# Kernel optimization log

Measured on AMD Instinct MI355X. Metric: run time of the kernel, lower is better.

The kernel has to match this reference:

```python
import jax, jax.numpy as jnp
import numpy as np

DIM = 512
NUM_HEADS = 8


def setup_inputs() -> dict:
    key = jax.random.key(0)
    k1, k2, k3, k4, k5 = jax.random.split(key, 5)
    B, N, C = 4, 4096, DIM
    x = jax.random.normal(k1, (B, N, C), dtype=jnp.float32)
    # Conv1d kernel_size=1 weights, squeezed to [out, in]
    qkv_w = jax.random.normal(k2, (3 * C, C), dtype=jnp.float32) * (C ** -0.5)
    qkv_b = jax.random.normal(k3, (3 * C,), dtype=jnp.float32) * 0.02
    out_w = jax.random.normal(k4, (C, C), dtype=jnp.float32) * (C ** -0.5)
    out_b = jax.random.normal(k5, (C,), dtype=jnp.float32) * 0.02
    return {"x": x, "qkv_w": qkv_w, "qkv_b": qkv_b, "out_w": out_w, "out_b": out_b}


def reference(x, qkv_w, qkv_b, out_w, out_b):
    B, N, C = x.shape
    H = NUM_HEADS
    hd = C // H
    scale = hd ** -0.5
    # 1x1 Conv1d == per-position linear: [B,N,C] x [3C,C] -> [B,N,3C]
    qkv = jnp.einsum('bnc,oc->bno', x, qkv_w) + qkv_b
    qkv = qkv.reshape(B, N, 3, H, hd)
    q, k, v = qkv[:, :, 0], qkv[:, :, 1], qkv[:, :, 2]  # each [B,N,H,hd]
    # NOTE: faithful to the original: q @ k.transpose(-2,-1) contracts head_dim
    # giving an [B,N,H,H] score matrix (attention across heads per position).
    scores = jnp.einsum('bnhd,bngd->bnhg', q, k) * scale
    attn = jax.nn.softmax(scores, axis=-1)
    out = jnp.einsum('bnhg,bngd->bnhd', attn, v)  # [B,N,H,hd]
    # Faithful to original: transpose(1,2) then reshape(B,N,C) interleaves axes.
    out = out.transpose(0, 2, 1, 3).reshape(B, N, C)
    out = jnp.einsum('bnc,oc->bno', out, out_w) + out_b
    return out
```

## Files before the change

### kernel.cpp

```cpp
#include <hip/hip_runtime.h>
#include <hip/hip_bf16.h>

#define DIMC 512
#define SEQ 4096
#define M_TOK 16384
#define N_QKV 1536

typedef __bf16 bfv8 __attribute__((ext_vector_type(8)));
typedef float f32v4 __attribute__((ext_vector_type(4)));
typedef unsigned short u16v8 __attribute__((ext_vector_type(8)));

#define VMCNT(n) asm volatile("s_waitcnt vmcnt(" #n ")" ::: "memory")
#define LGKM0()  asm volatile("s_waitcnt lgkmcnt(0)" ::: "memory")

static __device__ __forceinline__ float bf2f(unsigned short u) {
    union { unsigned int i; float f; } x; x.i = ((unsigned int)u) << 16; return x.f;
}
static __device__ __forceinline__ unsigned short f2bf(float f) {
    union { float f; unsigned int i; } x; x.f = f;
    unsigned int r = x.i + 0x7FFFu + ((x.i >> 16) & 1u);
    return (unsigned short)(r >> 16);
}

static __device__ __forceinline__ void gload_lds16(const void* g, void* s) {
    __builtin_amdgcn_global_load_lds(
        (const __attribute__((address_space(1))) unsigned int*)g,
        (__attribute__((address_space(3))) unsigned int*)s, 16, 0, 0);
}

#define NWQ8 (N_QKV * DIMC / 8)
#define NWO8 (DIMC * DIMC / 8)
__global__ __launch_bounds__(256) void cvt_w(
    const float* __restrict__ wq, const float* __restrict__ wo,
    unsigned short* __restrict__ wqb, unsigned short* __restrict__ wob)
{
    int i = blockIdx.x * 256 + threadIdx.x;
    const float* src; unsigned short* dst; int off;
    if (i < NWQ8) { src = wq; dst = wqb; off = i; }
    else          { src = wo; dst = wob; off = i - NWQ8; }
    const float4* p = (const float4*)src + (size_t)off * 2;
    float4 a = p[0], b = p[1];
    u16v8 o;
    o[0] = f2bf(a.x); o[1] = f2bf(a.y); o[2] = f2bf(a.z); o[3] = f2bf(a.w);
    o[4] = f2bf(b.x); o[5] = f2bf(b.y); o[6] = f2bf(b.z); o[7] = f2bf(b.w);
    *(u16v8*)(dst + (size_t)off * 8) = o;
}

__global__ __launch_bounds__(512) void gemm_qkv_f32a(
    const float* __restrict__ A,
    const unsigned short* __restrict__ B,
    const float* __restrict__ bias,
    unsigned short* __restrict__ Cout,
    int M, int N, int K)
{
    __shared__ __align__(16) unsigned short As[3][128 * 32];
    __shared__ __align__(16) unsigned short Bs[3][256 * 32];
    const int tid  = threadIdx.x;
    const int lane = tid & 63;
    const int wid  = tid >> 6;
    const int wm   = wid >> 2;
    const int wn   = wid & 3;
    const int m0 = blockIdx.x * 128;
    const int n0 = blockIdx.y * 256;
    const int frow = lane & 15;
    const int fcol = (lane >> 4) * 8;
    const int NT = K >> 5;

    f32v4 acc[4][4] = {};

    const int arow = wid * 16 + (lane & 15);
    const int ak0  = (lane >> 4) * 8;
    const float* aSrcF = A + (size_t)(m0 + arow) * K + ak0;
    const int aWidx = (arow * 32 + ak0) ^ (((arow >> 1) & 3) << 3);

    const unsigned short* bSrc[2];
    #pragma unroll
    for (int r = 0; r < 2; ++r) {
        const int brow = r * 128 + (tid >> 2);
        const int bcol = ((tid & 3) * 8) ^ (((brow >> 1) & 3) << 3);
        bSrc[r] = B + (size_t)(n0 + brow) * K + bcol;
    }
    const int bDst = wid * 512;

#define STAGE_B(kt, slot)                                                      \
    {                                                                          \
        gload_lds16(bSrc[0] + (kt) * 32, &Bs[slot][bDst]);                     \
        gload_lds16(bSrc[1] + (kt) * 32, &Bs[slot][4096 + bDst]);              \
    }
#define A_LOAD(kt, v0, v1)                                                     \
    { v0 = *(const float4*)(aSrcF + (kt) * 32);                                \
      v1 = *(const float4*)(aSrcF + (kt) * 32 + 4); }
#define A_WRITE(slot, v0, v1)                                                  \
    {                                                                          \
        u16v8 cv_;                                                             \
        cv_[0] = f2bf(v0.x); cv_[1] = f2bf(v0.y); cv_[2] = f2bf(v0.z);         \
        cv_[3] = f2bf(v0.w); cv_[4] = f2bf(v1.x); cv_[5] = f2bf(v1.y);         \
        cv_[6] = f2bf(v1.z); cv_[7] = f2bf(v1.w);                              \
        *(u16v8*)&As[slot][aWidx] = cv_;                                       \
    }

    float4 aC0, aC1, aN0, aN1, p00, p01, p10, p11;
    A_LOAD(0, p00, p01)
    A_LOAD(1, p10, p11)
    STAGE_B(0, 0)
    STAGE_B(1, 1)
    A_WRITE(0, p00, p01)
    A_WRITE(1, p10, p11)
    A_LOAD(2, aC0, aC1)
    VMCNT(4);
    LGKM0();
    __builtin_amdgcn_s_barrier();

    for (int t = 0; t < NT; ++t) {
        const int slot = t % 3;
        if (t + 3 < NT) A_LOAD(t + 3, aN0, aN1)
        if (t + 2 < NT) {
            STAGE_B(t + 2, (t + 2) % 3)
            A_WRITE((t + 2) % 3, aC0, aC1)
        }
        bfv8 af[4], bf[4];
        #pragma unroll
        for (int i = 0; i < 4; ++i) {
            const int r = wm * 64 + i * 16 + frow;
            af[i] = *(const bfv8*)(&As[slot][r * 32 + (fcol ^ (((r >> 1) & 3) << 3))]);
        }
        #pragma unroll
        for (int j = 0; j < 4; ++j) {
            const int r = wn * 64 + j * 16 + frow;
            bf[j] = *(const bfv8*)(&Bs[slot][r * 32 + (fcol ^ (((r >> 1) & 3) << 3))]);
        }
        LGKM0(); __builtin_amdgcn_sched_barrier(0);
        #pragma unroll
        for (int i = 0; i < 4; ++i)
            #pragma unroll
            for (int j = 0; j < 4; ++j)
                acc[i][j] = __builtin_amdgcn_mfma_f32_16x16x32_bf16(
                    af[i], bf[j], acc[i][j], 0, 0, 0);
        if (t + 2 < NT) { VMCNT(4); } else { VMCNT(0); }
        __builtin_amdgcn_s_barrier();
        aC0 = aN0; aC1 = aN1;
    }
#undef STAGE_B
#undef A_LOAD
#undef A_WRITE

    const int erow = (lane >> 4) * 4;
    const int ecol = lane & 15;
    #pragma unroll
    for (int j = 0; j < 4; ++j) {
        const int col = n0 + wn * 64 + j * 16 + ecol;
        const float bv = bias[col];
        #pragma unroll
        for (int i = 0; i < 4; ++i) {
            const int rbase = m0 + wm * 64 + i * 16 + erow;
            #pragma unroll
            for (int r = 0; r < 4; ++r)
                Cout[(size_t)(rbase + r) * N + col] = f2bf(acc[i][j][r] + bv);
        }
    }
}

__global__ __launch_bounds__(512) void gemm_nt_r3(
    const unsigned short* __restrict__ A,
    const unsigned short* __restrict__ B,
    const float* __restrict__ bias,
    float* __restrict__ Cout,
    int M, int N, int K)
{
    __shared__ __align__(16) unsigned short As[3][128 * 32];
    __shared__ __align__(16) unsigned short Bs[3][256 * 32];
    const int tid  = threadIdx.x;
    const int lane = tid & 63;
    const int wid  = tid >> 6;
    const int wm   = wid >> 2;
    const int wn   = wid & 3;
    const int m0 = blockIdx.x * 128;
    const int n0 = blockIdx.y * 256;
    const int frow = lane & 15;
    const int fcol = (lane >> 4) * 8;
    const int NT = K >> 5;

    f32v4 acc[4][4] = {};

    const int arow = tid >> 2;
    const int acol = ((tid & 3) * 8) ^ (((arow >> 1) & 3) << 3);
    const unsigned short* aSrc = A + (size_t)(m0 + arow) * K + acol;
    const unsigned short* bSrc[2];
    #pragma unroll
    for (int r = 0; r < 2; ++r) {
        const int brow = r * 128 + (tid >> 2);
        const int bcol = ((tid & 3) * 8) ^ (((brow >> 1) & 3) << 3);
        bSrc[r] = B + (size_t)(n0 + brow) * K + bcol;
    }
    const int aDst = wid * 512;

#define STAGE(kt, slot)                                                        \
    {                                                                          \
        gload_lds16(aSrc + (kt) * 32, &As[slot][aDst]);                        \
        gload_lds16(bSrc[0] + (kt) * 32, &Bs[slot][aDst]);                     \
        gload_lds16(bSrc[1] + (kt) * 32, &Bs[slot][4096 + aDst]);              \
    }

    STAGE(0, 0)
    STAGE(1, 1)
    VMCNT(3);
    __builtin_amdgcn_s_barrier();

    for (int t = 0; t < NT; ++t) {
        const int slot = t % 3;
        bfv8 af[4], bf[4];
        #pragma unroll
        for (int i = 0; i < 4; ++i) {
            const int r = wm * 64 + i * 16 + frow;
            af[i] = *(const bfv8*)(&As[slot][r * 32 + (fcol ^ (((r >> 1) & 3) << 3))]);
        }
        #pragma unroll
        for (int j = 0; j < 4; ++j) {
            const int r = wn * 64 + j * 16 + frow;
            bf[j] = *(const bfv8*)(&Bs[slot][r * 32 + (fcol ^ (((r >> 1) & 3) << 3))]);
        }
        if (t + 2 < NT) STAGE(t + 2, (t + 2) % 3)
        LGKM0(); __builtin_amdgcn_sched_barrier(0);
        #pragma unroll
        for (int i = 0; i < 4; ++i)
            #pragma unroll
            for (int j = 0; j < 4; ++j)
                acc[i][j] = __builtin_amdgcn_mfma_f32_16x16x32_bf16(
                    af[i], bf[j], acc[i][j], 0, 0, 0);
        if (t + 2 < NT) { VMCNT(3); } else { VMCNT(0); }
        __builtin_amdgcn_s_barrier();
    }
#undef STAGE

    const int erow = (lane >> 4) * 4;
    const int ecol = lane & 15;
    #pragma unroll
    for (int j = 0; j < 4; ++j) {
        const int col = n0 + wn * 64 + j * 16 + ecol;
        const float bv = bias[col];
        #pragma unroll
        for (int i = 0; i < 4; ++i) {
            const int rbase = m0 + wm * 64 + i * 16 + erow;
            #pragma unroll
            for (int r = 0; r < 4; ++r)
                Cout[(size_t)(rbase + r) * N + col] = acc[i][j][r] + bv;
        }
    }
}

__global__ __launch_bounds__(256) void attn_mix2(
    const unsigned short* __restrict__ Y1,
    unsigned short* __restrict__ Y2)
{
    const int tid  = threadIdx.x;
    const int tok  = blockIdx.x * 16 + (tid >> 4);
    const int l16  = tid & 15;
    const int h    = l16 >> 1;
    const int half = l16 & 1;
    const unsigned short* qkv = Y1 + (size_t)tok * N_QKV;

    float qf[32];
    #pragma unroll
    for (int c = 0; c < 4; ++c) {
        u16v8 v = *(const u16v8*)(qkv + h * 64 + half * 32 + c * 8);
        #pragma unroll
        for (int j = 0; j < 8; ++j) qf[c * 8 + j] = bf2f(v[j]);
    }
    float sc[8];
    #pragma unroll
    for (int g = 0; g < 8; ++g) {
        const unsigned short* kp = qkv + DIMC + g * 64 + half * 32;
        float a = 0.f;
        #pragma unroll
        for (int c = 0; c < 4; ++c) {
            u16v8 v = *(const u16v8*)(kp + c * 8);
            #pragma unroll
            for (int j = 0; j < 8; ++j) a = fmaf(qf[c * 8 + j], bf2f(v[j]), a);
        }
        a += __shfl_xor(a, 1);
        sc[g] = a * 0.125f;
    }
    float mx = sc[0];
    #pragma unroll
    for (int g = 1; g < 8; ++g) mx = fmaxf(mx, sc[g]);
    float sum = 0.f;
    #pragma unroll
    for (int g = 0; g < 8; ++g) { sc[g] = __expf(sc[g] - mx); sum += sc[g]; }
    const float inv = 1.f / sum;
    #pragma unroll
    for (int g = 0; g < 8; ++g) sc[g] *= inv;

    float o[32] = {};
    #pragma unroll
    for (int g = 0; g < 8; ++g) {
        const unsigned short* vp = qkv + 2 * DIMC + g * 64 + half * 32;
        #pragma unroll
        for (int c = 0; c < 4; ++c) {
            u16v8 v = *(const u16v8*)(vp + c * 8);
            #pragma unroll
            for (int j = 0; j < 8; ++j) o[c * 8 + j] = fmaf(sc[g], bf2f(v[j]), o[c * 8 + j]);
        }
    }
    const int n = tok & (SEQ - 1);
    const int b = tok >> 12;
    const size_t drow = (size_t)b * SEQ + h * 512 + (n >> 3);
    unsigned short* dst = Y2 + drow * DIMC + ((n & 7) << 6) + half * 32;
    #pragma unroll
    for (int c = 0; c < 4; ++c) {
        u16v8 ov;
        #pragma unroll
        for (int j = 0; j < 8; ++j) ov[j] = f2bf(o[c * 8 + j]);
        *(u16v8*)(dst + c * 8) = ov;
    }
}

extern "C" void kernel_launch(void* const* d_in, const int* in_sizes, int n_in,
                              void* d_out, int out_size, void* d_ws, size_t ws_size,
                              hipStream_t stream) {
    const float* x     = (const float*)d_in[0];
    const float* qkv_w = (const float*)d_in[1];
    const float* qkv_b = (const float*)d_in[2];
    const float* out_w = (const float*)d_in[3];
    const float* out_b = (const float*)d_in[4];
    float* out = (float*)d_out;

    unsigned short* Y1 = (unsigned short*)d_ws;
    unsigned short* Y2 = Y1 + (size_t)M_TOK * N_QKV;
    unsigned short* Wq = Y2 + (size_t)M_TOK * DIMC;
    unsigned short* Wo = Wq + (size_t)N_QKV * DIMC;

    cvt_w<<<(NWQ8 + NWO8) / 256, 256, 0, stream>>>(qkv_w, out_w, Wq, Wo);

    gemm_qkv_f32a<<<dim3(M_TOK / 128, N_QKV / 256), 512, 0, stream>>>(
        x, Wq, qkv_b, Y1, M_TOK, N_QKV, DIMC);

    attn_mix2<<<M_TOK / 16, 256, 0, stream>>>(Y1, Y2);

    gemm_nt_r3<<<dim3(M_TOK / 128, DIMC / 256), 512, 0, stream>>>(
        Y2, Wo, out_b, out, M_TOK, DIMC, DIMC);
}
```

Before: 98.41 us.

## Stage fp32 A tiles directly to LDS via async loads, convert after read

The QKV GEMM now stages the fp32 activation tile straight into LDS with direct global-to-LDS loads, using an XOR swizzle, instead of loading into registers, converting to bf16 and writing to LDS. Conversion to bf16 moves to after the LDS fragment reads, just before the MFMAs. This removes register staging, the conversion from the load path, and the separate LDS writes. In exchange it doubles LDS footprint and LDS read traffic for A and adds per-iteration conversion work in the compute loop. Rounding also changes from a manual round-to-nearest-even routine to the compiler's bf16 cast.

Measured after the change: 86.89 us. -11.7%, faster.

```diff
diff --git a/kernel.cpp b/kernel.cpp
--- a/kernel.cpp
+++ b/kernel.cpp
@@ -53,7 +53,7 @@
     unsigned short* __restrict__ Cout,
     int M, int N, int K)
 {
-    __shared__ __align__(16) unsigned short As[3][128 * 32];
+    __shared__ __align__(16) float          AsF[3][128 * 32];
     __shared__ __align__(16) unsigned short Bs[3][256 * 32];
     const int tid  = threadIdx.x;
     const int lane = tid & 63;
@@ -68,11 +68,13 @@
 
     f32v4 acc[4][4] = {};
 
-    const int arow = wid * 16 + (lane & 15);
-    const int ak0  = (lane >> 4) * 8;
-    const float* aSrcF = A + (size_t)(m0 + arow) * K + ak0;
-    const int aWidx = (arow * 32 + ak0) ^ (((arow >> 1) & 3) << 3);
-
+    const float* aSrcG[2];
+    #pragma unroll
+    for (int s = 0; s < 2; ++s) {
+        const int row = (s * 512 + tid) >> 3;
+        const int g   = tid & 7;
+        aSrcG[s] = A + (size_t)(m0 + row) * K + ((g ^ (row & 7)) << 2);
+    }
     const unsigned short* bSrc[2];
     #pragma unroll
     for (int r = 0; r < 2; ++r) {
@@ -81,55 +83,50 @@
         bSrc[r] = B + (size_t)(n0 + brow) * K + bcol;
     }
     const int bDst = wid * 512;
-
-#define STAGE_B(kt, slot)                                                      \
+    const int aDstF = wid * 256;
+
+#define STAGE(kt, slot)                                                        \
     {                                                                          \
+        gload_lds16(aSrcG[0] + (kt) * 32, &AsF[slot][aDstF]);                  \
+        gload_lds16(aSrcG[1] + (kt) * 32, &AsF[slot][2048 + aDstF]);           \
         gload_lds16(bSrc[0] + (kt) * 32, &Bs[slot][bDst]);                     \
         gload_lds16(bSrc[1] + (kt) * 32, &Bs[slot][4096 + bDst]);              \
     }
-#define A_LOAD(kt, v0, v1)                                                     \
-    { v0 = *(const float4*)(aSrcF + (kt) * 32);                                \
-      v1 = *(const float4*)(aSrcF + (kt) * 32 + 4); }
-#define A_WRITE(slot, v0, v1)                                                  \
-    {                                                                          \
-        u16v8 cv_;                                                             \
-        cv_[0] = f2bf(v0.x); cv_[1] = f2bf(v0.y); cv_[2] = f2bf(v0.z);         \
-        cv_[3] = f2bf(v0.w); cv_[4] = f2bf(v1.x); cv_[5] = f2bf(v1.y);         \
-        cv_[6] = f2bf(v1.z); cv_[7] = f2bf(v1.w);                              \
-        *(u16v8*)&As[slot][aWidx] = cv_;                                       \
-    }
-
-    float4 aC0, aC1, aN0, aN1, p00, p01, p10, p11;
-    A_LOAD(0, p00, p01)
-    A_LOAD(1, p10, p11)
-    STAGE_B(0, 0)
-    STAGE_B(1, 1)
-    A_WRITE(0, p00, p01)
-    A_WRITE(1, p10, p11)
-    A_LOAD(2, aC0, aC1)
+
+    STAGE(0, 0)
+    STAGE(1, 1)
     VMCNT(4);
-    LGKM0();
     __builtin_amdgcn_s_barrier();
 
     for (int t = 0; t < NT; ++t) {
         const int slot = t % 3;
-        if (t + 3 < NT) A_LOAD(t + 3, aN0, aN1)
-        if (t + 2 < NT) {
-            STAGE_B(t + 2, (t + 2) % 3)
-            A_WRITE((t + 2) % 3, aC0, aC1)
-        }
-        bfv8 af[4], bf[4];
+        f32v4 alo[4], ahi[4];
         #pragma unroll
         for (int i = 0; i < 4; ++i) {
             const int r = wm * 64 + i * 16 + frow;
-            af[i] = *(const bfv8*)(&As[slot][r * 32 + (fcol ^ (((r >> 1) & 3) << 3))]);
-        }
+            const int m = r & 7;
+            const int g0 = (lane >> 4) * 2;
+            alo[i] = *(const f32v4*)(&AsF[slot][r * 32 + ((g0 ^ m) << 2)]);
+            ahi[i] = *(const f32v4*)(&AsF[slot][r * 32 + (((g0 + 1) ^ m) << 2)]);
+        }
+        bfv8 bf[4];
         #pragma unroll
         for (int j = 0; j < 4; ++j) {
             const int r = wn * 64 + j * 16 + frow;
             bf[j] = *(const bfv8*)(&Bs[slot][r * 32 + (fcol ^ (((r >> 1) & 3) << 3))]);
         }
+        if (t + 2 < NT) STAGE(t + 2, (t + 2) % 3)
         LGKM0(); __builtin_amdgcn_sched_barrier(0);
+        bfv8 af[4];
+        #pragma unroll
+        for (int i = 0; i < 4; ++i) {
+            bfv8 v;
+            v[0] = (__bf16)alo[i][0]; v[1] = (__bf16)alo[i][1];
+            v[2] = (__bf16)alo[i][2]; v[3] = (__bf16)alo[i][3];
+            v[4] = (__bf16)ahi[i][0]; v[5] = (__bf16)ahi[i][1];
+            v[6] = (__bf16)ahi[i][2]; v[7] = (__bf16)ahi[i][3];
+            af[i] = v;
+        }
         #pragma unroll
         for (int i = 0; i < 4; ++i)
             #pragma unroll
@@ -138,11 +135,8 @@
                     af[i], bf[j], acc[i][j], 0, 0, 0);
         if (t + 2 < NT) { VMCNT(4); } else { VMCNT(0); }
         __builtin_amdgcn_s_barrier();
-        aC0 = aN0; aC1 = aN1;
-    }
-#undef STAGE_B
-#undef A_LOAD
-#undef A_WRITE
+    }
+#undef STAGE
 
     const int erow = (lane >> 4) * 4;
     const int ecol = lane & 15;
```
